# Kernel tuning notes

Measured on AMD Instinct MI355X. Metric: run time of the kernel, lower is better.

## Reference

```python
import jax, jax.numpy as jnp
import numpy as np

N, D, E, R = 50000, 128, 640000, 500
BN_EPS = 1e-3  # keras BatchNormalization default
L2_EPS = 1e-12  # tf.nn.l2_normalize default


def setup_inputs() -> dict:
    key = jax.random.key(0)
    ks = jax.random.split(key, 10)
    rows = jnp.sort(jax.random.randint(ks[0], (E,), 0, N, dtype=jnp.int32))
    cols = jax.random.randint(ks[1], (E,), 0, N, dtype=jnp.int32)
    return {
        "x": jax.random.normal(ks[2], (N, D), dtype=jnp.float32),
        "rows": rows,
        "cols": cols,
        "adj_vals": jax.random.uniform(ks[3], (E,), dtype=jnp.float32),
        "rel_ids": jax.random.randint(ks[4], (E,), 0, R, dtype=jnp.int32),
        "gamma1": jnp.ones((D,), jnp.float32),
        "beta1": jnp.zeros((D,), jnp.float32),
        "mean1": jnp.zeros((D,), jnp.float32),
        "var1": jnp.ones((D,), jnp.float32),
        "W1": jax.random.normal(ks[5], (D, D), dtype=jnp.float32) * 0.05,
        "b1": jnp.zeros((D,), jnp.float32),
        "gamma2": jnp.ones((D,), jnp.float32),
        "beta2": jnp.zeros((D,), jnp.float32),
        "mean2": jnp.zeros((D,), jnp.float32),
        "var2": jnp.ones((D,), jnp.float32),
        "relation_coeffs": jax.random.uniform(ks[6], (R,), dtype=jnp.float32),
        "coeff_kernel": jax.random.normal(ks[7], (N, 1), dtype=jnp.float32) * 0.05,
        "Wd": jax.random.normal(ks[8], (D, D), dtype=jnp.float32) * 0.05,
        "bd": jnp.zeros((D,), jnp.float32),
    }


def _bn(h, gamma, beta, mean, var):
    # keras BatchNormalization, inference mode (moving stats)
    return (h - mean) * jax.lax.rsqrt(var + BN_EPS) * gamma + beta


def _spmm(vals, rows, cols, h, n):
    # sparse [n,n] @ dense [n,d]: gather source rows, weight, scatter-add to dest
    return jax.ops.segment_sum(vals[:, None] * h[cols], rows, num_segments=n)


def _l2n(a):
    # tf.nn.l2_normalize(a, axis=1)
    sq = jnp.sum(a * a, axis=1, keepdims=True)
    return a * jax.lax.rsqrt(jnp.maximum(sq, L2_EPS))


def reference(x, rows, cols, adj_vals, rel_ids,
              gamma1, beta1, mean1, var1, W1, b1,
              gamma2, beta2, mean2, var2,
              relation_coeffs, coeff_kernel, Wd, bd):
    n = x.shape[0]
    # ---- agg1: alinet_gcn: tanh(A @ (BN(x) @ W1) + b1) ----
    h = _bn(x, gamma1, beta1, mean1, var1)
    y1 = jnp.tanh(_spmm(adj_vals, rows, cols, h @ W1, n) + b1)
    # ---- agg2: Rgin ----
    h2 = _bn(y1, gamma2, beta2, mean2, var2)
    # relation-weighted edge values: A.values / (rel_coeffs[values] + 1)
    ev = adj_vals / (relation_coeffs[rel_ids] + 1.0)
    agg = _spmm(ev, rows, cols, h2, n)
    self_term = h2 * (coeff_kernel + 1.0)  # CoeffLayer(mul=True)
    y2 = (agg + self_term) @ Wd + bd       # Dense(dim)
    # ---- output: concat of per-layer l2-normalized embeddings, renormalized ----
    y = jnp.concatenate([_l2n(x), _l2n(y1), _l2n(y2)], axis=1)
    return _l2n(y)
```

## Files before the change

### kernel.cpp

```cpp
#include <hip/hip_runtime.h>
#include <math.h>

#define D 128
#define BN_EPS 1e-3f
#define L2_EPS 1e-12f

typedef unsigned int uint;
typedef unsigned short ushort;
typedef __attribute__((ext_vector_type(8))) short bf16x8;
typedef __attribute__((ext_vector_type(4))) float f32x4;

__device__ __forceinline__ ushort f2bf(float f) {
  uint u = __float_as_uint(f);
  uint r = (u + 0x7fffu + ((u >> 16) & 1u)) >> 16;
  return (ushort)r;
}
__device__ __forceinline__ float bflo(uint u) { return __uint_as_float(u << 16); }
__device__ __forceinline__ float bfhi(uint u) { return __uint_as_float(u & 0xffff0000u); }
__device__ __forceinline__ float bf2f(ushort h) { return __uint_as_float(((uint)h) << 16); }

__device__ __forceinline__ void pack_bfrag_block(
    const float* __restrict__ W, const float* __restrict__ gamma,
    const float* __restrict__ var, ushort* __restrict__ Bf, int blk, int tid) {
  int t = blk * 256 + tid;
  int f = t >> 6, lane = t & 63;
  int kc = f >> 3, nt = f & 7, q = lane >> 4, m = lane & 15;
  ushort tmp[8];
#pragma unroll
  for (int j = 0; j < 8; ++j) {
    int k = kc * 32 + q * 8 + j;
    float s = gamma[k] * rsqrtf(var[k] + BN_EPS);
    tmp[j] = f2bf(s * W[k * D + nt * 16 + m]);
  }
  uint4 o;
  o.x = (uint)tmp[0] | ((uint)tmp[1] << 16);
  o.y = (uint)tmp[2] | ((uint)tmp[3] << 16);
  o.z = (uint)tmp[4] | ((uint)tmp[5] << 16);
  o.w = (uint)tmp[6] | ((uint)tmp[7] << 16);
  reinterpret_cast<uint4*>(Bf)[t] = o;
}

__device__ __forceinline__ void bn_bias_block(
    const float* __restrict__ W, const float* __restrict__ gamma,
    const float* __restrict__ beta, const float* __restrict__ mean,
    const float* __restrict__ var, float* __restrict__ outb, int j) {
  float acc = 0.f;
  for (int k = 0; k < D; ++k) {
    float s = gamma[k] * rsqrtf(var[k] + BN_EPS);
    float sh = beta[k] - mean[k] * s;
    acc += sh * W[k * D + j];
  }
  outb[j] = acc;
}

__global__ __launch_bounds__(256) void prep_kernel(
    const float* __restrict__ x, ushort* __restrict__ xbf, int n4,
    const int* __restrict__ rows, int* __restrict__ row_ptr, int n, int e,
    const float* __restrict__ W1, const float* __restrict__ g1,
    const float* __restrict__ v1, ushort* __restrict__ Bf1,
    const float* __restrict__ Wd, const float* __restrict__ g2,
    const float* __restrict__ v2, ushort* __restrict__ Bf2,
    const float* __restrict__ beta1, const float* __restrict__ mean1,
    float* __restrict__ bnb,
    const float* __restrict__ beta2, const float* __restrict__ mean2,
    float* __restrict__ shd,
    const float* __restrict__ relc, float* __restrict__ recip, int nrel,
    int nbConv, int nbRp) {
  const int b = blockIdx.x, tid = threadIdx.x;
  if (b < nbConv) {
    int i = b * 256 + tid;
    if (i < n4) {
      float4 v = reinterpret_cast<const float4*>(x)[i];
      ushort4 o;
      o.x = f2bf(v.x); o.y = f2bf(v.y); o.z = f2bf(v.z); o.w = f2bf(v.w);
      reinterpret_cast<ushort4*>(xbf)[i] = o;
    }
    return;
  }
  int bb = b - nbConv;
  if (bb < nbRp) {
    int i = bb * 256 + tid;
    if (i <= n) {
      int lo = 0, hi = e;
      while (lo < hi) {
        int mid = (lo + hi) >> 1;
        if (rows[mid] < i) lo = mid + 1; else hi = mid;
      }
      row_ptr[i] = lo;
    }
    return;
  }
  bb -= nbRp;
  if (bb < 8) { pack_bfrag_block(W1, g1, v1, Bf1, bb, tid); return; }
  if (bb < 16) { pack_bfrag_block(Wd, g2, v2, Bf2, bb - 8, tid); return; }
  if (bb == 16) { if (tid < D) bn_bias_block(W1, g1, beta1, mean1, v1, bnb, tid); return; }
  if (bb == 17) { if (tid < D) bn_bias_block(Wd, g2, beta2, mean2, v2, shd, tid); return; }
  int i = (bb - 18) * 256 + tid;
  if (i < nrel) recip[i] = 1.0f / (relc[i] + 1.0f);
}

template <bool REL, bool SELF>
__global__ __launch_bounds__(256) void spmm_kernel(
    const ushort* __restrict__ src, const int* __restrict__ row_ptr,
    const int* __restrict__ cols, const float* __restrict__ vals,
    const int* __restrict__ rel_ids, const float* __restrict__ recip,
    const float* __restrict__ ck, ushort* __restrict__ outA,
    float* __restrict__ rowsum, int n) {
  const int wave = threadIdx.x >> 6, lane = threadIdx.x & 63;
  const int r = blockIdx.x * 4 + wave;
  if (r >= n) return;
  const uint* S = reinterpret_cast<const uint*>(src);
  const int e0 = row_ptr[r], e1 = row_ptr[r + 1];
  const int last = e1 - 1;
  float a0 = 0.f, a1 = 0.f, b0 = 0.f, b1 = 0.f, ws = 0.f;
  for (int base = e0; base < e1; base += 8) {
    int c[8]; float w[8];
#pragma unroll
    for (int u = 0; u < 8; ++u) {
      int ee = base + u;
      int eC = ee < last ? ee : last;
      c[u] = cols[eC];
      float wv = vals[eC];
      if (REL) wv *= recip[rel_ids[eC]];
      w[u] = (ee <= last) ? wv : 0.f;
    }
    uint g[8];
#pragma unroll
    for (int u = 0; u < 8; ++u) g[u] = S[(size_t)c[u] * 64 + lane];
#pragma unroll
    for (int u = 0; u < 8; u += 2) {
      a0 = fmaf(w[u], bflo(g[u]), a0);
      a1 = fmaf(w[u], bfhi(g[u]), a1);
      b0 = fmaf(w[u + 1], bflo(g[u + 1]), b0);
      b1 = fmaf(w[u + 1], bfhi(g[u + 1]), b1);
      ws += w[u] + w[u + 1];
    }
  }
  if (SELF) {
    uint us = S[(size_t)r * 64 + lane];
    float cp = ck[r] + 1.0f;
    a0 = fmaf(cp, bflo(us), a0);
    a1 = fmaf(cp, bfhi(us), a1);
  }
  a0 += b0; a1 += b1;
  reinterpret_cast<uint*>(outA)[(size_t)r * 64 + lane] =
      (uint)f2bf(a0) | ((uint)f2bf(a1) << 16);
  if (lane == 0) rowsum[r] = ws;
}

__global__ __launch_bounds__(256) void gemm1_mfma_kernel(
    const ushort* __restrict__ A, const ushort* __restrict__ Bf,
    const float* __restrict__ bnb, const float* __restrict__ b1,
    const float* __restrict__ rs1, ushort* __restrict__ y1, int M) {
  const int wave = threadIdx.x >> 6, lane = threadIdx.x & 63;
  const int row0 = blockIdx.x * 64 + wave * 16;
  if (row0 >= M) return;
  const int m = lane & 15, q = lane >> 4;
  const int row = row0 + m;
  const int arow = row < M ? row : M - 1;

  const bf16x8* Av = reinterpret_cast<const bf16x8*>(A);
  const bf16x8* Bv = reinterpret_cast<const bf16x8*>(Bf);

  bf16x8 af[4];
#pragma unroll
  for (int kc = 0; kc < 4; ++kc) af[kc] = Av[(size_t)arow * 16 + kc * 4 + q];

  f32x4 acc[8];
#pragma unroll
  for (int nt = 0; nt < 8; ++nt) acc[nt] = (f32x4){0.f, 0.f, 0.f, 0.f};

#pragma unroll
  for (int kc = 0; kc < 4; ++kc) {
#pragma unroll
    for (int nt = 0; nt < 8; ++nt) {
      bf16x8 b = Bv[(kc * 8 + nt) * 64 + lane];
      acc[nt] = __builtin_amdgcn_mfma_f32_16x16x32_bf16(b, af[kc], acc[nt], 0, 0, 0);
    }
  }

  if (row < M) {
    float rs = rs1[row];
#pragma unroll
    for (int nt = 0; nt < 8; ++nt) {
      const float4 bn = *reinterpret_cast<const float4*>(&bnb[nt * 16 + q * 4]);
      const float4 bb = *reinterpret_cast<const float4*>(&b1[nt * 16 + q * 4]);
      ushort4 o;
      o.x = f2bf(tanhf(acc[nt][0] + rs * bn.x + bb.x));
      o.y = f2bf(tanhf(acc[nt][1] + rs * bn.y + bb.y));
      o.z = f2bf(tanhf(acc[nt][2] + rs * bn.z + bb.z));
      o.w = f2bf(tanhf(acc[nt][3] + rs * bn.w + bb.w));
      *reinterpret_cast<ushort4*>(&y1[(size_t)row * D + nt * 16 + q * 4]) = o;
    }
  }
}

__global__ __launch_bounds__(256) void gemm2_fused_kernel(
    const ushort* __restrict__ A2, const ushort* __restrict__ Bf,
    const float* __restrict__ shd, const float* __restrict__ bd,
    const float* __restrict__ rs2, const float* __restrict__ ck,
    const float* __restrict__ x, const ushort* __restrict__ y1,
    float* __restrict__ out, int M) {
  const int wave = threadIdx.x >> 6, lane = threadIdx.x & 63;
  const int row0 = blockIdx.x * 64 + wave * 16;
  if (row0 >= M) return;
  const int m = lane & 15, q = lane >> 4;
  const int row = row0 + m;
  const int arow = row < M ? row : M - 1;

  const bf16x8* Av = reinterpret_cast<const bf16x8*>(A2);
  const bf16x8* Bv = reinterpret_cast<const bf16x8*>(Bf);

  bf16x8 af[4];
#pragma unroll
  for (int kc = 0; kc < 4; ++kc) af[kc] = Av[(size_t)arow * 16 + kc * 4 + q];

  f32x4 acc[8];
#pragma unroll
  for (int nt = 0; nt < 8; ++nt) acc[nt] = (f32x4){0.f, 0.f, 0.f, 0.f};

#pragma unroll
  for (int kc = 0; kc < 4; ++kc) {
#pragma unroll
    for (int nt = 0; nt < 8; ++nt) {
      bf16x8 b = Bv[(kc * 8 + nt) * 64 + lane];
      acc[nt] = __builtin_amdgcn_mfma_f32_16x16x32_bf16(b, af[kc], acc[nt], 0, 0, 0);
    }
  }

  const float rb = rs2[arow] + ck[arow] + 1.0f;
  float4 xv[8];
  ushort4 y1v[8];
  float s0 = 0.f, s1 = 0.f, s2 = 0.f;
#pragma unroll
  for (int nt = 0; nt < 8; ++nt) {
    const float4 sh = *reinterpret_cast<const float4*>(&shd[nt * 16 + q * 4]);
    const float4 bb = *reinterpret_cast<const float4*>(&bd[nt * 16 + q * 4]);
    acc[nt][0] += rb * sh.x + bb.x;
    acc[nt][1] += rb * sh.y + bb.y;
    acc[nt][2] += rb * sh.z + bb.z;
    acc[nt][3] += rb * sh.w + bb.w;
    s2 += acc[nt][0] * acc[nt][0] + acc[nt][1] * acc[nt][1] +
          acc[nt][2] * acc[nt][2] + acc[nt][3] * acc[nt][3];
    xv[nt] = *reinterpret_cast<const float4*>(&x[(size_t)arow * D + nt * 16 + q * 4]);
    s0 += xv[nt].x * xv[nt].x + xv[nt].y * xv[nt].y +
          xv[nt].z * xv[nt].z + xv[nt].w * xv[nt].w;
    y1v[nt] = *reinterpret_cast<const ushort4*>(&y1[(size_t)arow * D + nt * 16 + q * 4]);
    float ya = bf2f(y1v[nt].x), yb = bf2f(y1v[nt].y);
    float yc = bf2f(y1v[nt].z), yd = bf2f(y1v[nt].w);
    s1 += ya * ya + yb * yb + yc * yc + yd * yd;
  }
  s0 += __shfl_xor(s0, 16); s0 += __shfl_xor(s0, 32);
  s1 += __shfl_xor(s1, 16); s1 += __shfl_xor(s1, 32);
  s2 += __shfl_xor(s2, 16); s2 += __shfl_xor(s2, 32);
  const float i0 = 1.0f / sqrtf(fmaxf(s0, L2_EPS));
  const float i1 = 1.0f / sqrtf(fmaxf(s1, L2_EPS));
  const float i2 = 1.0f / sqrtf(fmaxf(s2, L2_EPS));
  const float tot = s0 * i0 * i0 + s1 * i1 * i1 + s2 * i2 * i2;
  const float sc = 1.0f / sqrtf(fmaxf(tot, L2_EPS));
  const float f0 = i0 * sc, f1 = i1 * sc, f2 = i2 * sc;

  if (row < M) {
    float* orow = out + (size_t)row * 384;
#pragma unroll
    for (int nt = 0; nt < 8; ++nt) {
      const int c = nt * 16 + q * 4;
      float4 ox = make_float4(xv[nt].x * f0, xv[nt].y * f0, xv[nt].z * f0, xv[nt].w * f0);
      float4 oy = make_float4(bf2f(y1v[nt].x) * f1, bf2f(y1v[nt].y) * f1,
                              bf2f(y1v[nt].z) * f1, bf2f(y1v[nt].w) * f1);
      float4 oz = make_float4(acc[nt][0] * f2, acc[nt][1] * f2,
                              acc[nt][2] * f2, acc[nt][3] * f2);
      *reinterpret_cast<float4*>(orow + c) = ox;
      *reinterpret_cast<float4*>(orow + 128 + c) = oy;
      *reinterpret_cast<float4*>(orow + 256 + c) = oz;
    }
  }
}

extern "C" void kernel_launch(void* const* d_in, const int* in_sizes, int n_in,
                              void* d_out, int out_size, void* d_ws, size_t ws_size,
                              hipStream_t stream) {
  const float* x      = (const float*)d_in[0];
  const int*   rows   = (const int*)d_in[1];
  const int*   cols   = (const int*)d_in[2];
  const float* adj    = (const float*)d_in[3];
  const int*   rel    = (const int*)d_in[4];
  const float* gamma1 = (const float*)d_in[5];
  const float* beta1  = (const float*)d_in[6];
  const float* mean1  = (const float*)d_in[7];
  const float* var1   = (const float*)d_in[8];
  const float* W1     = (const float*)d_in[9];
  const float* b1     = (const float*)d_in[10];
  const float* gamma2 = (const float*)d_in[11];
  const float* beta2  = (const float*)d_in[12];
  const float* mean2  = (const float*)d_in[13];
  const float* var2   = (const float*)d_in[14];
  const float* relc   = (const float*)d_in[15];
  const float* ck     = (const float*)d_in[16];
  const float* Wd     = (const float*)d_in[17];
  const float* bd     = (const float*)d_in[18];
  float* out = (float*)d_out;

  const int n = in_sizes[0] / D;
  const int e = in_sizes[1];
  const int nrel = in_sizes[15];
  size_t nd = (size_t)n * D;

  ushort* xbf   = (ushort*)d_ws;
  ushort* y1bf  = xbf + nd;
  ushort* aggbf = y1bf + nd;
  ushort* Bf1   = aggbf + nd;
  ushort* Bf2   = Bf1 + 16384;
  float*  bnb   = (float*)(Bf2 + 16384);
  float*  shd   = bnb + D;
  float*  rs1   = shd + D;
  float*  rs2   = rs1 + n;
  float*  recip = rs2 + n;
  int* row_ptr  = (int*)(recip + nrel);

  const int n4 = (int)(nd / 4);
  const int nbConv = (n4 + 255) / 256;
  const int nbRp = (n + 1 + 255) / 256;
  const int nbRecip = (nrel + 255) / 256;
  const int nbPrep = nbConv + nbRp + 18 + nbRecip;

  prep_kernel<<<nbPrep, 256, 0, stream>>>(
      x, xbf, n4, rows, row_ptr, n, e,
      W1, gamma1, var1, Bf1, Wd, gamma2, var2, Bf2,
      beta1, mean1, bnb, beta2, mean2, shd,
      relc, recip, nrel, nbConv, nbRp);

  int sblocks = (n + 3) / 4;
  int gblocks = (n + 63) / 64;

  spmm_kernel<false, false><<<sblocks, 256, 0, stream>>>(
      xbf, row_ptr, cols, adj, nullptr, nullptr, nullptr, aggbf, rs1, n);
  gemm1_mfma_kernel<<<gblocks, 256, 0, stream>>>(aggbf, Bf1, bnb, b1, rs1, y1bf, n);
  spmm_kernel<true, true><<<sblocks, 256, 0, stream>>>(
      y1bf, row_ptr, cols, adj, rel, recip, ck, aggbf, rs2, n);
  gemm2_fused_kernel<<<gblocks, 256, 0, stream>>>(
      aggbf, Bf2, shd, bd, rs2, ck, x, y1bf, out, n);
}
```

Baseline: 258.3 us.

## Pack edge metadata and process four rows per wave in SpMM

Prep now builds packed (col, weight) edge arrays for both layers, with the relation-scaled weight computed once per edge. This replaces separate cols/vals/rel_ids/recip loads inside the SpMM. The SpMM kernel is restructured so each wave handles four rows with 16 lanes per row, each lane loading 16 bytes (8 bf16). This cuts metadata loads per row and widens the gather loads, aiming to improve memory efficiency. The cost is extra prep work and workspace for two E-sized arrays, plus divergence when rows in a wave have unequal lengths (the loop runs to the max length).

Result: faster. 229.3 us (-11.2%).

```diff
diff --git a/kernel.cpp b/kernel.cpp
--- a/kernel.cpp
+++ b/kernel.cpp
@@ -64,7 +64,9 @@
     float* __restrict__ bnb,
     const float* __restrict__ beta2, const float* __restrict__ mean2,
     float* __restrict__ shd,
-    const float* __restrict__ relc, float* __restrict__ recip, int nrel,
+    const int* __restrict__ cols, const float* __restrict__ adj,
+    const int* __restrict__ rel, const float* __restrict__ relc,
+    uint2* __restrict__ ew1, uint2* __restrict__ ew2,
     int nbConv, int nbRp) {
   const int b = blockIdx.x, tid = threadIdx.x;
   if (b < nbConv) {
@@ -96,56 +98,85 @@
   if (bb == 16) { if (tid < D) bn_bias_block(W1, g1, beta1, mean1, v1, bnb, tid); return; }
   if (bb == 17) { if (tid < D) bn_bias_block(Wd, g2, beta2, mean2, v2, shd, tid); return; }
   int i = (bb - 18) * 256 + tid;
-  if (i < nrel) recip[i] = 1.0f / (relc[i] + 1.0f);
-}
-
-template <bool REL, bool SELF>
-__global__ __launch_bounds__(256) void spmm_kernel(
+  if (i < e) {
+    uint c = (uint)cols[i];
+    float a = adj[i];
+    ew1[i] = make_uint2(c, __float_as_uint(a));
+    float w2 = a / (relc[rel[i]] + 1.0f);
+    ew2[i] = make_uint2(c, __float_as_uint(w2));
+  } else if (i == e) {
+    ew1[i] = make_uint2(0u, 0u);
+    ew2[i] = make_uint2(0u, 0u);
+  }
+}
+
+template <bool SELF>
+__global__ __launch_bounds__(256) void spmm4_kernel(
     const ushort* __restrict__ src, const int* __restrict__ row_ptr,
-    const int* __restrict__ cols, const float* __restrict__ vals,
-    const int* __restrict__ rel_ids, const float* __restrict__ recip,
-    const float* __restrict__ ck, ushort* __restrict__ outA,
-    float* __restrict__ rowsum, int n) {
-  const int wave = threadIdx.x >> 6, lane = threadIdx.x & 63;
-  const int r = blockIdx.x * 4 + wave;
+    const uint2* __restrict__ ew, const float* __restrict__ ck,
+    ushort* __restrict__ outA, float* __restrict__ rowsum, int n) {
+  const int lane = threadIdx.x & 63;
+  const int g = lane >> 4, m = lane & 15;
+  const int r = blockIdx.x * 16 + (threadIdx.x >> 6) * 4 + g;
+  const int rr = r < n ? r : n - 1;
+  const int e0 = row_ptr[rr];
+  int len = row_ptr[rr + 1] - e0;
+  if (r >= n) len = 0;
+  int mx = len;
+  mx = max(mx, __shfl_xor(mx, 16));
+  mx = max(mx, __shfl_xor(mx, 32));
+  const int lastOff = len > 0 ? len - 1 : 0;
+
+  const uint4* S4 = reinterpret_cast<const uint4*>(src);
+  float acc[8] = {0.f, 0.f, 0.f, 0.f, 0.f, 0.f, 0.f, 0.f};
+  float ws = 0.f;
+
+  for (int i = 0; i < mx; i += 4) {
+    uint2 md[4];
+    uint4 gv[4];
+#pragma unroll
+    for (int u = 0; u < 4; ++u) {
+      int ii = i + u;
+      int off = ii < len ? ii : lastOff;
+      md[u] = ew[e0 + off];
+    }
+#pragma unroll
+    for (int u = 0; u < 4; ++u) gv[u] = S4[(size_t)md[u].x * 16 + m];
+#pragma unroll
+    for (int u = 0; u < 4; ++u) {
+      float w = (i + u) < len ? __uint_as_float(md[u].y) : 0.f;
+      ws += w;
+      acc[0] = fmaf(w, bflo(gv[u].x), acc[0]);
+      acc[1] = fmaf(w, bfhi(gv[u].x), acc[1]);
+      acc[2] = fmaf(w, bflo(gv[u].y), acc[2]);
+      acc[3] = fmaf(w, bfhi(gv[u].y), acc[3]);
+      acc[4] = fmaf(w, bflo(gv[u].z), acc[4]);
+      acc[5] = fmaf(w, bfhi(gv[u].z), acc[5]);
+      acc[6] = fmaf(w, bflo(gv[u].w), acc[6]);
+      acc[7] = fmaf(w, bfhi(gv[u].w), acc[7]);
+    }
+  }
+
   if (r >= n) return;
-  const uint* S = reinterpret_cast<const uint*>(src);
-  const int e0 = row_ptr[r], e1 = row_ptr[r + 1];
-  const int last = e1 - 1;
-  float a0 = 0.f, a1 = 0.f, b0 = 0.f, b1 = 0.f, ws = 0.f;
-  for (int base = e0; base < e1; base += 8) {
-    int c[8]; float w[8];
-#pragma unroll
-    for (int u = 0; u < 8; ++u) {
-      int ee = base + u;
-      int eC = ee < last ? ee : last;
-      c[u] = cols[eC];
-      float wv = vals[eC];
-      if (REL) wv *= recip[rel_ids[eC]];
-      w[u] = (ee <= last) ? wv : 0.f;
-    }
-    uint g[8];
-#pragma unroll
-    for (int u = 0; u < 8; ++u) g[u] = S[(size_t)c[u] * 64 + lane];
-#pragma unroll
-    for (int u = 0; u < 8; u += 2) {
-      a0 = fmaf(w[u], bflo(g[u]), a0);
-      a1 = fmaf(w[u], bfhi(g[u]), a1);
-      b0 = fmaf(w[u + 1], bflo(g[u + 1]), b0);
-      b1 = fmaf(w[u + 1], bfhi(g[u + 1]), b1);
-      ws += w[u] + w[u + 1];
-    }
-  }
   if (SELF) {
-    uint us = S[(size_t)r * 64 + lane];
-    float cp = ck[r] + 1.0f;
-    a0 = fmaf(cp, bflo(us), a0);
-    a1 = fmaf(cp, bfhi(us), a1);
-  }
-  a0 += b0; a1 += b1;
-  reinterpret_cast<uint*>(outA)[(size_t)r * 64 + lane] =
-      (uint)f2bf(a0) | ((uint)f2bf(a1) << 16);
-  if (lane == 0) rowsum[r] = ws;
+    uint4 us = S4[(size_t)rr * 16 + m];
+    float cp = ck[rr] + 1.0f;
+    acc[0] = fmaf(cp, bflo(us.x), acc[0]);
+    acc[1] = fmaf(cp, bfhi(us.x), acc[1]);
+    acc[2] = fmaf(cp, bflo(us.y), acc[2]);
+    acc[3] = fmaf(cp, bfhi(us.y), acc[3]);
+    acc[4] = fmaf(cp, bflo(us.z), acc[4]);
+    acc[5] = fmaf(cp, bfhi(us.z), acc[5]);
+    acc[6] = fmaf(cp, bflo(us.w), acc[6]);
+    acc[7] = fmaf(cp, bfhi(us.w), acc[7]);
+  }
+  uint4 o;
+  o.x = (uint)f2bf(acc[0]) | ((uint)f2bf(acc[1]) << 16);
+  o.y = (uint)f2bf(acc[2]) | ((uint)f2bf(acc[3]) << 16);
+  o.z = (uint)f2bf(acc[4]) | ((uint)f2bf(acc[5]) << 16);
+  o.w = (uint)f2bf(acc[6]) | ((uint)f2bf(acc[7]) << 16);
+  reinterpret_cast<uint4*>(outA)[(size_t)r * 16 + m] = o;
+  if (m == 0) rowsum[r] = ws;
 }
 
 __global__ __launch_bounds__(256) void gemm1_mfma_kernel(
@@ -303,41 +334,43 @@
 
   const int n = in_sizes[0] / D;
   const int e = in_sizes[1];
-  const int nrel = in_sizes[15];
   size_t nd = (size_t)n * D;
 
-  ushort* xbf   = (ushort*)d_ws;
-  ushort* y1bf  = xbf + nd;
-  ushort* aggbf = y1bf + nd;
-  ushort* Bf1   = aggbf + nd;
-  ushort* Bf2   = Bf1 + 16384;
-  float*  bnb   = (float*)(Bf2 + 16384);
-  float*  shd   = bnb + D;
-  float*  rs1   = shd + D;
-  float*  rs2   = rs1 + n;
-  float*  recip = rs2 + n;
-  int* row_ptr  = (int*)(recip + nrel);
+  char* p = (char*)d_ws;
+  ushort* xbf   = (ushort*)p; p += nd * 2;
+  ushort* y1bf  = (ushort*)p; p += nd * 2;
+  ushort* aggbf = (ushort*)p; p += nd * 2;
+  ushort* Bf1   = (ushort*)p; p += 32768;
+  ushort* Bf2   = (ushort*)p; p += 32768;
+  float*  bnb   = (float*)p;  p += 512;
+  float*  shd   = (float*)p;  p += 512;
+  float*  rs1   = (float*)p;  p += (size_t)n * 4;
+  float*  rs2   = (float*)p;  p += (size_t)n * 4;
+  p = (char*)(((uintptr_t)p + 15) & ~(uintptr_t)15);
+  uint2* ew1    = (uint2*)p;  p += (size_t)(e + 1) * 8;
+  uint2* ew2    = (uint2*)p;  p += (size_t)(e + 1) * 8;
+  int* row_ptr  = (int*)p;    p += (size_t)(n + 1) * 4;
 
   const int n4 = (int)(nd / 4);
   const int nbConv = (n4 + 255) / 256;
   const int nbRp = (n + 1 + 255) / 256;
-  const int nbRecip = (nrel + 255) / 256;
-  const int nbPrep = nbConv + nbRp + 18 + nbRecip;
+  const int nbEw = (e + 1 + 255) / 256;
+  const int nbPrep = nbConv + nbRp + 18 + nbEw;
 
   prep_kernel<<<nbPrep, 256, 0, stream>>>(
       x, xbf, n4, rows, row_ptr, n, e,
       W1, gamma1, var1, Bf1, Wd, gamma2, var2, Bf2,
       beta1, mean1, bnb, beta2, mean2, shd,
-      relc, recip, nrel, nbConv, nbRp);
-
-  int sblocks = (n + 3) / 4;
+      cols, adj, rel, relc, ew1, ew2, nbConv, nbRp);
+
+  int sblocks = (n + 15) / 16;
   int gblocks = (n + 63) / 64;
 
-  spmm_kernel<false, false><<<sblocks, 256, 0, stream>>>(
-      xbf, row_ptr, cols, adj, nullptr, nullptr, nullptr, aggbf, rs1, n);
+  spmm4_kernel<false><<<sblocks, 256, 0, stream>>>(
+      xbf, row_ptr, ew1, nullptr, aggbf, rs1, n);
   gemm1_mfma_kernel<<<gblocks, 256, 0, stream>>>(aggbf, Bf1, bnb, b1, rs1, y1bf, n);
-  spmm_kernel<true, true><<<sblocks, 256, 0, stream>>>(
-      y1bf, row_ptr, cols, adj, rel, recip, ck, aggbf, rs2, n);
+  spmm4_kernel<true><<<sblocks, 256, 0, stream>>>(
+      y1bf, row_ptr, ew2, ck, aggbf, rs2, n);
   gemm2_fused_kernel<<<gblocks, 256, 0, stream>>>(
       aggbf, Bf2, shd, bd, rs2, ck, x, y1bf, out, n);
 }
```
